# Optimization experiments

Measured on AMD Instinct MI355X. Metric: run time of the kernel, lower is better.

The kernel has to match this reference:

```python
import jax, jax.numpy as jnp
import numpy as np

BITS = 8
EPS = 1e-08


def _scalar_quantize_maxabs(x, scale, bits, eps):
    # clamp(round(x / scale), -qmax, qmax) with a fixed (precomputed) scalar scale
    qmax = float(2 ** (bits - 1) - 1)
    s = jnp.maximum(scale, eps)
    return jnp.clip(jnp.round(x / s), -qmax, qmax)


def setup_inputs() -> dict:
    key = jax.random.key(0)
    k1, k2, k3 = jax.random.split(key, 3)
    B, S, D_in, D_out = 4, 2048, 2048, 2048
    hidden_states = jax.random.normal(k1, (B, S, D_in), dtype=jnp.float32)
    # weight_quantized holds low-bit integer values stored as float (as produced by the quantizer)
    qmax = float(2 ** (BITS - 1) - 1)
    weight_quantized = jnp.round(
        jnp.clip(jax.random.normal(k2, (D_in, D_out), dtype=jnp.float32) * (qmax / 3.0), -qmax, qmax)
    )
    x_scale = jnp.asarray(0.05, dtype=jnp.float32)
    bias = jax.random.normal(k3, (D_out,), dtype=jnp.float32)
    return {
        "hidden_states": hidden_states,
        "weight_quantized": weight_quantized,
        "x_scale": x_scale,
        "bias": bias,
    }


def reference(hidden_states, weight_quantized, x_scale, bias) -> jnp.ndarray:
    original_shape = hidden_states.shape[:-1]
    input_dim = hidden_states.shape[-1]
    x_flat = hidden_states.reshape(-1, input_dim)  # [B*S, D_in]
    x_q = _scalar_quantize_maxabs(x_flat, x_scale.reshape(()), BITS, EPS)
    out = x_q.astype(weight_quantized.dtype) @ weight_quantized  # [B*S, D_out]
    out = out + bias.astype(out.dtype)[None, :]
    return out.astype(hidden_states.dtype).reshape(*original_shape, weight_quantized.shape[1])
```

## Files before the change

### kernel.cpp

```cpp
#include <hip/hip_runtime.h>
#include <cstdint>
#include <cstddef>

#define MDIM 8192
#define NDIM 2048
#define KDIM 2048

constexpr int BM = 128, BN = 128, BK = 64;

typedef int v4i __attribute__((ext_vector_type(4)));

__device__ __forceinline__ void async_ld16(const void* g, void* l) {
    __builtin_amdgcn_global_load_lds(
        (const __attribute__((address_space(1))) int*)g,
        (__attribute__((address_space(3))) int*)l,
        16, 0, 0);
}

__device__ __forceinline__ uint32_t q8(float x, float inv) {
    float q = fminf(fmaxf(rintf(x * inv), -127.f), 127.f);
    return (uint32_t)((int)q) & 0xffu;
}

#define WBLOCKS ((KDIM / 64) * (NDIM / 64))
#define XBLOCKS 2048
#define XSTRIDE (XBLOCKS * 256)
#define XITERS  (MDIM * KDIM / 4 / XSTRIDE)

__global__ void quant_kernel(const float4* __restrict__ x, uint32_t* __restrict__ xq,
                             const float* __restrict__ scale_p,
                             const float* __restrict__ w, uint32_t* __restrict__ wt) {
    __shared__ uint32_t t[64][17];
    const int tid = threadIdx.x;

    if (blockIdx.x >= WBLOCKS) {
        int i = (blockIdx.x - WBLOCKS) * 256 + tid;
        float inv = 1.0f / fmaxf(scale_p[0], 1e-8f);
#pragma unroll
        for (int k = 0; k < XITERS; ++k) {
            float4 v = x[i + k * XSTRIDE];
            xq[i + k * XSTRIDE] =
                q8(v.x, inv) | (q8(v.y, inv) << 8) | (q8(v.z, inv) << 16) | (q8(v.w, inv) << 24);
        }
        return;
    }

    const int bid = blockIdx.x;
    const int k0 = (bid >> 5) * 64;
    const int n0 = (bid & 31) * 64;
    const int rr  = tid >> 4;
    const int c4  = (tid & 15) * 4;
#pragma unroll
    for (int p = 0; p < 4; ++p) {
        int r = rr + p * 16;
        float4 v = *(const float4*)&w[(size_t)(k0 + r) * NDIM + n0 + c4];
        uint32_t pk = (uint32_t)((int)rintf(v.x) & 0xff)
                    | ((uint32_t)((int)rintf(v.y) & 0xff) << 8)
                    | ((uint32_t)((int)rintf(v.z) & 0xff) << 16)
                    | ((uint32_t)((int)rintf(v.w) & 0xff) << 24);
        t[r][c4 >> 2] = pk;
    }
    __syncthreads();
#pragma unroll
    for (int p = 0; p < 4; ++p) {
        int c = rr + p * 16;
        uint32_t o = 0;
#pragma unroll
        for (int j = 0; j < 4; ++j) {
            uint32_t b = (t[c4 + j][c >> 2] >> ((c & 3) * 8)) & 0xffu;
            o |= b << (j * 8);
        }
        wt[((size_t)(n0 + c) * KDIM + k0 + c4) >> 2] = o;
    }
}

__global__ __launch_bounds__(256, 4)
void gemm_i8_kernel(const int8_t* __restrict__ A,
                    const int8_t* __restrict__ Bt,
                    const float* __restrict__ bias,
                    float* __restrict__ C) {
    __shared__ alignas(16) int8_t lA[2][BM * BK];
    __shared__ alignas(16) int8_t lB[2][BN * BK];

    const int tid  = threadIdx.x;
    const int lane = tid & 63;
    const int wave = tid >> 6;
    const int wm   = wave & 1;
    const int wn   = wave >> 1;
    const int m0   = blockIdx.y * BM;
    const int n0   = blockIdx.x * BN;

    const int srow = lane >> 2;
    const int schk = (lane & 3) ^ ((srow >> 1) & 3);
    const int8_t* gA = A  + (size_t)(m0 + wave * 32 + srow) * KDIM + schk * 16;
    const int8_t* gB = Bt + (size_t)(n0 + wave * 32 + srow) * KDIM + schk * 16;
    const int lwo = wave * 2048;

    const int quad = lane >> 4;
    const int lr   = lane & 15;
    const int fchk = (quad ^ ((lr >> 1) & 3)) * 16;
    const int aoff = (wm * 64 + lr) * BK + fchk;
    const int boff = (wn * 64 + lr) * BK + fchk;

    v4i acc[4][4];
#pragma unroll
    for (int i = 0; i < 4; ++i)
#pragma unroll
        for (int j = 0; j < 4; ++j)
            acc[i][j] = (v4i){0, 0, 0, 0};

#define STAGE(buf, kof)                                                        \
    do {                                                                       \
        async_ld16(gA + (kof), &lA[buf][lwo]);                                 \
        async_ld16(gA + (kof) + (size_t)16 * KDIM, &lA[buf][lwo + 1024]);      \
        async_ld16(gB + (kof), &lB[buf][lwo]);                                 \
        async_ld16(gB + (kof) + (size_t)16 * KDIM, &lB[buf][lwo + 1024]);      \
    } while (0)

#define COMPUTE(buf)                                                           \
    do {                                                                       \
        v4i af[4], bf[4];                                                      \
        _Pragma("unroll")                                                      \
        for (int i = 0; i < 4; ++i)                                            \
            af[i] = *(const v4i*)&lA[buf][aoff + i * 16 * BK];                 \
        _Pragma("unroll")                                                      \
        for (int j = 0; j < 4; ++j)                                            \
            bf[j] = *(const v4i*)&lB[buf][boff + j * 16 * BK];                 \
        _Pragma("unroll")                                                      \
        for (int i = 0; i < 4; ++i)                                            \
            _Pragma("unroll")                                                  \
            for (int j = 0; j < 4; ++j)                                        \
                acc[i][j] = __builtin_amdgcn_mfma_i32_16x16x64_i8(             \
                    af[i], bf[j], acc[i][j], 0, 0, 0);                         \
    } while (0)

    STAGE(0, 0);
    int kof = BK;
    for (int it = 0; it < KDIM / BK - 1; ++it) {
        __syncthreads();
        STAGE((it + 1) & 1, kof);
        kof += BK;
        COMPUTE(it & 1);
    }
    __syncthreads();
    COMPUTE((KDIM / BK - 1) & 1);

    const int crow = m0 + wm * 64 + quad * 4;
    const int ccol = n0 + wn * 64 + lr;
    float bj[4];
#pragma unroll
    for (int j = 0; j < 4; ++j) bj[j] = bias[ccol + j * 16];
#pragma unroll
    for (int i = 0; i < 4; ++i)
#pragma unroll
        for (int j = 0; j < 4; ++j)
#pragma unroll
            for (int r = 0; r < 4; ++r)
                C[(size_t)(crow + i * 16 + r) * NDIM + (ccol + j * 16)] = (float)acc[i][j][r] + bj[j];
}

extern "C" void kernel_launch(void* const* d_in, const int* in_sizes, int n_in,
                              void* d_out, int out_size, void* d_ws, size_t ws_size,
                              hipStream_t stream) {
    const float* x    = (const float*)d_in[0];
    const float* w    = (const float*)d_in[1];
    const float* xs   = (const float*)d_in[2];
    const float* bias = (const float*)d_in[3];
    float* out = (float*)d_out;

    int8_t* xq = (int8_t*)d_ws;
    int8_t* wt = xq + (size_t)MDIM * KDIM;

    quant_kernel<<<WBLOCKS + XBLOCKS, 256, 0, stream>>>(
        (const float4*)x, (uint32_t*)xq, xs, w, (uint32_t*)wt);
    gemm_i8_kernel<<<dim3(NDIM / BN, MDIM / BM), 256, 0, stream>>>(xq, wt, bias, out);
}
```

Before: 168.9 us.

## Widen GEMM tile to 128x256 with 8 waves and XCD-aware block remapping

Doubles the GEMM block's N tile to 256 and the block size to 512 threads (8 waves), splitting the A and B staging loads across the waves. The goal is to cut global and LDS traffic per MFMA through greater operand reuse. Blocks are remapped so each XCD gets a contiguous band of M rows, improving L2 locality. The x quantization loop now uses four contiguous chunks instead of a grid stride. The risks are a larger LDS footprint (48 KB per block), lower occupancy, and possible register pressure from the aggressive launch_bounds hint.

```diff
diff --git a/kernel.cpp b/kernel.cpp
--- a/kernel.cpp
+++ b/kernel.cpp
@@ -6,7 +6,7 @@
 #define NDIM 2048
 #define KDIM 2048
 
-constexpr int BM = 128, BN = 128, BK = 64;
+constexpr int BM = 128, BN = 256, BK = 64;
 
 typedef int v4i __attribute__((ext_vector_type(4)));
 
@@ -23,9 +23,8 @@
 }
 
 #define WBLOCKS ((KDIM / 64) * (NDIM / 64))
-#define XBLOCKS 2048
-#define XSTRIDE (XBLOCKS * 256)
-#define XITERS  (MDIM * KDIM / 4 / XSTRIDE)
+#define XCHUNK (MDIM * KDIM / 4 / 4)
+#define XBLOCKS (XCHUNK / 256)
 
 __global__ void quant_kernel(const float4* __restrict__ x, uint32_t* __restrict__ xq,
                              const float* __restrict__ scale_p,
@@ -37,9 +36,9 @@
         int i = (blockIdx.x - WBLOCKS) * 256 + tid;
         float inv = 1.0f / fmaxf(scale_p[0], 1e-8f);
 #pragma unroll
-        for (int k = 0; k < XITERS; ++k) {
-            float4 v = x[i + k * XSTRIDE];
-            xq[i + k * XSTRIDE] =
+        for (int k = 0; k < 4; ++k) {
+            float4 v = x[i + k * XCHUNK];
+            xq[i + k * XCHUNK] =
                 q8(v.x, inv) | (q8(v.y, inv) << 8) | (q8(v.z, inv) << 16) | (q8(v.w, inv) << 24);
         }
         return;
@@ -74,7 +73,7 @@
     }
 }
 
-__global__ __launch_bounds__(256, 4)
+__global__ __launch_bounds__(512, 6)
 void gemm_i8_kernel(const int8_t* __restrict__ A,
                     const int8_t* __restrict__ Bt,
                     const float* __restrict__ bias,
@@ -87,14 +86,19 @@
     const int wave = tid >> 6;
     const int wm   = wave & 1;
     const int wn   = wave >> 1;
-    const int m0   = blockIdx.y * BM;
-    const int n0   = blockIdx.x * BN;
+
+    const int bidlin = blockIdx.y * gridDim.x + blockIdx.x;
+    const int xcd    = bidlin & 7;
+    const int idx    = bidlin >> 3;
+    const int m0     = (xcd * 8 + (idx >> 3)) * BM;
+    const int n0     = (idx & 7) * BN;
 
     const int srow = lane >> 2;
     const int schk = (lane & 3) ^ ((srow >> 1) & 3);
-    const int8_t* gA = A  + (size_t)(m0 + wave * 32 + srow) * KDIM + schk * 16;
+    const int8_t* gA = A  + (size_t)(m0 + wave * 16 + srow) * KDIM + schk * 16;
     const int8_t* gB = Bt + (size_t)(n0 + wave * 32 + srow) * KDIM + schk * 16;
-    const int lwo = wave * 2048;
+    const int lwoA = wave * 1024;
+    const int lwoB = wave * 2048;
 
     const int quad = lane >> 4;
     const int lr   = lane & 15;
@@ -111,10 +115,9 @@
 
 #define STAGE(buf, kof)                                                        \
     do {                                                                       \
-        async_ld16(gA + (kof), &lA[buf][lwo]);                                 \
-        async_ld16(gA + (kof) + (size_t)16 * KDIM, &lA[buf][lwo + 1024]);      \
-        async_ld16(gB + (kof), &lB[buf][lwo]);                                 \
-        async_ld16(gB + (kof) + (size_t)16 * KDIM, &lB[buf][lwo + 1024]);      \
+        async_ld16(gA + (kof), &lA[buf][lwoA]);                                \
+        async_ld16(gB + (kof), &lB[buf][lwoB]);                                \
+        async_ld16(gB + (kof) + (size_t)16 * KDIM, &lB[buf][lwoB + 1024]);     \
     } while (0)
 
 #define COMPUTE(buf)                                                           \
@@ -122,10 +125,10 @@
         v4i af[4], bf[4];                                                      \
         _Pragma("unroll")                                                      \
         for (int i = 0; i < 4; ++i)                                            \
-            af[i] = *(const v4i*)&lA[buf][aoff + i * 16 * BK];                 \
+            af[i] = *(const v4i*)&lA[buf][aoff + i * 1024];                    \
         _Pragma("unroll")                                                      \
         for (int j = 0; j < 4; ++j)                                            \
-            bf[j] = *(const v4i*)&lB[buf][boff + j * 16 * BK];                 \
+            bf[j] = *(const v4i*)&lB[buf][boff + j * 1024];                    \
         _Pragma("unroll")                                                      \
         for (int i = 0; i < 4; ++i)                                            \
             _Pragma("unroll")                                                  \
@@ -173,5 +176,5 @@
 
     quant_kernel<<<WBLOCKS + XBLOCKS, 256, 0, stream>>>(
         (const float4*)x, (uint32_t*)xq, xs, w, (uint32_t*)wt);
-    gemm_i8_kernel<<<dim3(NDIM / BN, MDIM / BM), 256, 0, stream>>>(xq, wt, bias, out);
+    gemm_i8_kernel<<<dim3(NDIM / BN, MDIM / BM), 512, 0, stream>>>(xq, wt, bias, out);
 }
```

New measurement: 382.9 us. +126.7%, slower.
